# Kernel optimization log

Measured on AMD Instinct MI355X. Metric: run time of the kernel, lower is better.

## Reference

```python
import jax, jax.numpy as jnp
import numpy as np

B, N = 512, 256

def setup_inputs() -> dict:
    key = jax.random.key(0)
    k1, k2 = jax.random.split(key)
    D1 = jax.random.normal(k1, (B, N, N), dtype=jnp.float32)
    D2 = jax.random.normal(k2, (B, N, N), dtype=jnp.float32)
    types1 = jnp.zeros((B, N), dtype=jnp.int32)
    types2 = jnp.zeros((B, N), dtype=jnp.int32)
    return {"D1": D1, "D2": D2, "types1": types1, "types2": types2}


def reference(D1, D2, types1, types2):
    # Hungarian cost: cost[b, i, j] = |mean_k D1[b, k, i] - mean_k D2[b, k, j]|.
    # For an absolute-difference cost between two scalar profiles, the optimal
    # linear assignment (what scipy's linear_sum_assignment returns inside the
    # original tf.py_function) matches sorted values to sorted values; with a
    # point-type constraint, it matches sorted values within each type group.
    # We therefore compute the exact optimal permutation via a lexicographic
    # sort on (type, mean-distance) for each side, which is fully vectorized
    # and avoids the host-side CPU loop of the original layer.
    a = jnp.mean(D1, axis=1)  # [B, N] column means of D1
    b = jnp.mean(D2, axis=1)  # [B, N]

    def optimal_perm(a_row, b_row, t1, t2):
        # sort primarily by type, secondarily by value (lexsort: last key primary)
        order1 = jnp.lexsort((a_row, t1))  # [N] atom indices of D1 in sorted order
        order2 = jnp.lexsort((b_row, t2))  # [N] target positions in sorted order
        # atom order1[k] is placed at position order2[k]
        return jnp.zeros_like(order1).at[order2].set(order1)  # perm[j] = source atom for slot j

    perm = jax.vmap(optimal_perm)(a, b, types1, types2)  # [B, N]

    # Symmetric reorder of rows and columns of D1 by perm.
    D1_rows = jnp.take_along_axis(D1, perm[:, :, None], axis=1)          # [B, N, N]
    D1_reordered = jnp.take_along_axis(D1_rows, perm[:, None, :], axis=2)  # [B, N, N]
    types1_reordered = jnp.take_along_axis(types1, perm, axis=1)         # [B, N]

    # The original layer applies tf.stop_gradient to both outputs.
    D1_reordered = jax.lax.stop_gradient(D1_reordered)
    types1_reordered = jax.lax.stop_gradient(types1_reordered)
    return D1_reordered, types1_reordered
```

## Files before the change

kernel.cpp:

```cpp
#include <hip/hip_runtime.h>
#include <hip/hip_bf16.h>

#define BATCH 512
#define NN 256

__device__ __forceinline__ float4 f4add(float4 x, float4 y) {
  return make_float4(x.x + y.x, x.y + y.y, x.z + y.z, x.w + y.w);
}

__global__ __launch_bounds__(512, 4) void fused_hungarian_kernel(
    const float* __restrict__ D1, const float* __restrict__ D2,
    const int* __restrict__ t1, const int* __restrict__ t2,
    float* __restrict__ out, float* __restrict__ types_out) {
  const int b = blockIdx.x;
  const int tid = threadIdx.x;

  __shared__ float4 partial4[2][4][64];
  __shared__ float va[NN], vb[NN];
  __shared__ int ta[NN], tb[NN];
  __shared__ int ord1[NN], ord2[NN], plds[NN];
  __shared__ float4 rows[8][64];

  {
    const int c4 = tid & 63;
    const int slot = tid >> 6;
    const int mat = slot >> 2;
    const int s2 = slot & 3;
    const int h = s2 >> 1;
    const int tq = s2 & 1;
    const float* __restrict__ src = (mat ? D2 : D1) + (size_t)b * (NN * NN);
    const float* cb = src + (size_t)(h * 128 + 4 * tq) * NN + 4 * c4;

    float4 r0 = *(const float4*)(cb + (size_t)0 * NN);
    float4 r1 = *(const float4*)(cb + (size_t)1 * NN);
    float4 r2 = *(const float4*)(cb + (size_t)2 * NN);
    float4 r3 = *(const float4*)(cb + (size_t)3 * NN);
#pragma unroll
    for (int m = 1; m < 16; ++m) {
      const float* p = cb + (size_t)(8 * m) * NN;
      r0 = f4add(r0, *(const float4*)(p + (size_t)0 * NN));
      r1 = f4add(r1, *(const float4*)(p + (size_t)1 * NN));
      r2 = f4add(r2, *(const float4*)(p + (size_t)2 * NN));
      r3 = f4add(r3, *(const float4*)(p + (size_t)3 * NN));
    }
    partial4[mat][s2][c4] = f4add(f4add(r0, r1), f4add(r2, r3));
  }
  if (tid < NN) ta[tid] = t1[b * NN + tid];
  else          tb[tid - NN] = t2[b * NN + (tid - NN)];
  __syncthreads();

  {
    const int mat = tid >> 8;
    const int c = tid & 255;
    const float p0 = ((const float*)partial4[mat][0])[c];
    const float p1 = ((const float*)partial4[mat][1])[c];
    const float p2 = ((const float*)partial4[mat][2])[c];
    const float p3 = ((const float*)partial4[mat][3])[c];
    const float tot = (p0 + p1) + (p2 + p3);
    const float mean = tot * (1.0f / 256.0f);
    if (mat == 0) va[c] = mean; else vb[c] = mean;
  }
  __syncthreads();

  {
    const int side = tid >> 8;
    const int c = tid & 255;
    const float* __restrict__ vv = side ? vb : va;
    const int* __restrict__ tt = side ? tb : ta;
    const float vi = vv[c];
    const int ti = tt[c];
    int r = 0;
#pragma unroll 4
    for (int j = 0; j < NN; ++j) {
      const int tj = tt[j];
      const float vj = vv[j];
      const bool less =
          (tj < ti) || (tj == ti && (vj < vi || (vj == vi && j < c)));
      r += less ? 1 : 0;
    }
    if (side == 0) ord1[r] = c;
    else           ord2[r] = c;
  }
  __syncthreads();
  if (tid < NN) plds[ord2[tid]] = ord1[tid];
  __syncthreads();
  if (tid < NN) types_out[b * NN + tid] = (float)ta[plds[tid]];

  {
    const int w = tid >> 6;
    const int lane = tid & 63;
    const int j0 = 4 * lane;
    const int pj0 = plds[j0 + 0];
    const int pj1 = plds[j0 + 1];
    const int pj2 = plds[j0 + 2];
    const int pj3 = plds[j0 + 3];
    const float* __restrict__ Db = D1 + (size_t)b * (NN * NN);
    float* __restrict__ outb = out + (size_t)b * (NN * NN);
    const float* rowf = (const float*)&rows[w][0];

    int pi = plds[w];
    float4 vst = *(const float4*)(Db + (size_t)pi * NN + j0);
    for (int iter = 0; iter < 32; ++iter) {
      const int i = iter * 8 + w;
      rows[w][lane] = vst;
      if (iter < 31) {
        const int pin = plds[(iter + 1) * 8 + w];
        vst = *(const float4*)(Db + (size_t)pin * NN + j0);
      }
      float4 o;
      o.x = rowf[pj0];
      o.y = rowf[pj1];
      o.z = rowf[pj2];
      o.w = rowf[pj3];
      *(float4*)(outb + (size_t)i * NN + j0) = o;
    }
  }
}

extern "C" void kernel_launch(void* const* d_in, const int* in_sizes, int n_in,
                              void* d_out, int out_size, void* d_ws, size_t ws_size,
                              hipStream_t stream) {
  const float* D1 = (const float*)d_in[0];
  const float* D2 = (const float*)d_in[1];
  const int* t1 = (const int*)d_in[2];
  const int* t2 = (const int*)d_in[3];

  float* out = (float*)d_out;
  float* types_out = out + (size_t)BATCH * NN * NN;

  fused_hungarian_kernel<<<BATCH, 512, 0, stream>>>(D1, D2, t1, t2, out,
                                                    types_out);
}
```

Before: 346.0 us.

## Stage column-sum loads via global_load_lds DMA and deepen gather prefetch

```diff
diff --git a/kernel.cpp b/kernel.cpp
--- a/kernel.cpp
+++ b/kernel.cpp
@@ -1,11 +1,18 @@
 #include <hip/hip_runtime.h>
-#include <hip/hip_bf16.h>
 
 #define BATCH 512
 #define NN 256
 
+typedef __attribute__((ext_vector_type(4))) float f32x4;
+
 __device__ __forceinline__ float4 f4add(float4 x, float4 y) {
   return make_float4(x.x + y.x, x.y + y.y, x.z + y.z, x.w + y.w);
+}
+
+__device__ __forceinline__ void dma_row16(const float* g, float* l) {
+  __builtin_amdgcn_global_load_lds(
+      (const __attribute__((address_space(1))) void*)g,
+      (__attribute__((address_space(3))) void*)l, 16, 0, 0);
 }
 
 __global__ __launch_bounds__(512, 4) void fused_hungarian_kernel(
@@ -14,51 +21,75 @@
     float* __restrict__ out, float* __restrict__ types_out) {
   const int b = blockIdx.x;
   const int tid = threadIdx.x;
+  const int lane = tid & 63;
+  const int wv = tid >> 6;
 
-  __shared__ float4 partial4[2][4][64];
-  __shared__ float va[NN], vb[NN];
-  __shared__ int ta[NN], tb[NN];
-  __shared__ int ord1[NN], ord2[NN], plds[NN];
-  __shared__ float4 rows[8][64];
+  __shared__ __align__(16) char smem[73728];
+  float* const stagef = (float*)smem;
+  float* const va = (float*)smem;
+  float* const vb = (float*)(smem + 1024);
+  int* const ta = (int*)(smem + 2048);
+  int* const tb = (int*)(smem + 3072);
+  int* const ord1 = (int*)(smem + 4096);
+  int* const ord2 = (int*)(smem + 5120);
+  int* const plds = (int*)(smem + 6144);
+  float4* const rows = (float4*)(smem + 8192);
+  float* const partialf = (float*)(smem + 65536);
 
   {
-    const int c4 = tid & 63;
-    const int slot = tid >> 6;
-    const int mat = slot >> 2;
-    const int s2 = slot & 3;
+    const int mat = wv >> 2;
+    const int s2 = wv & 3;
     const int h = s2 >> 1;
     const int tq = s2 & 1;
     const float* __restrict__ src = (mat ? D2 : D1) + (size_t)b * (NN * NN);
-    const float* cb = src + (size_t)(h * 128 + 4 * tq) * NN + 4 * c4;
+    const float* cb = src + (size_t)(h * 128 + 4 * tq) * NN;
+    float* const wstage = stagef + wv * 2048;
 
-    float4 r0 = *(const float4*)(cb + (size_t)0 * NN);
-    float4 r1 = *(const float4*)(cb + (size_t)1 * NN);
-    float4 r2 = *(const float4*)(cb + (size_t)2 * NN);
-    float4 r3 = *(const float4*)(cb + (size_t)3 * NN);
 #pragma unroll
-    for (int m = 1; m < 16; ++m) {
-      const float* p = cb + (size_t)(8 * m) * NN;
-      r0 = f4add(r0, *(const float4*)(p + (size_t)0 * NN));
-      r1 = f4add(r1, *(const float4*)(p + (size_t)1 * NN));
-      r2 = f4add(r2, *(const float4*)(p + (size_t)2 * NN));
-      r3 = f4add(r3, *(const float4*)(p + (size_t)3 * NN));
+    for (int mk = 0; mk < 8; ++mk) {
+      const int m = mk >> 2, k = mk & 3;
+      dma_row16(cb + (size_t)(8 * m + k) * NN + 4 * lane,
+                wstage + ((m & 1) * 4 + k) * 256);
     }
-    partial4[mat][s2][c4] = f4add(f4add(r0, r1), f4add(r2, r3));
+
+    float4 r0, r1, r2, r3;
+#pragma unroll
+    for (int m = 0; m < 16; ++m) {
+      if (m == 15) asm volatile("s_waitcnt vmcnt(0)" ::: "memory");
+      else         asm volatile("s_waitcnt vmcnt(4)" ::: "memory");
+      const float* sp = wstage + (m & 1) * 1024 + 4 * lane;
+      const float4 v0 = *(const float4*)(sp + 0);
+      const float4 v1 = *(const float4*)(sp + 256);
+      const float4 v2 = *(const float4*)(sp + 512);
+      const float4 v3 = *(const float4*)(sp + 768);
+      asm volatile("s_waitcnt lgkmcnt(0)" ::: "memory");
+      if (m + 2 < 16) {
+#pragma unroll
+        for (int k = 0; k < 4; ++k)
+          dma_row16(cb + (size_t)(8 * (m + 2) + k) * NN + 4 * lane,
+                    wstage + ((m & 1) * 4 + k) * 256);
+      }
+      if (m == 0) { r0 = v0; r1 = v1; r2 = v2; r3 = v3; }
+      else {
+        r0 = f4add(r0, v0); r1 = f4add(r1, v1);
+        r2 = f4add(r2, v2); r3 = f4add(r3, v3);
+      }
+    }
+    const float4 part = f4add(f4add(r0, r1), f4add(r2, r3));
+    *(float4*)(partialf + (mat * 4 + s2) * 256 + 4 * lane) = part;
   }
-  if (tid < NN) ta[tid] = t1[b * NN + tid];
-  else          tb[tid - NN] = t2[b * NN + (tid - NN)];
   __syncthreads();
 
   {
     const int mat = tid >> 8;
     const int c = tid & 255;
-    const float p0 = ((const float*)partial4[mat][0])[c];
-    const float p1 = ((const float*)partial4[mat][1])[c];
-    const float p2 = ((const float*)partial4[mat][2])[c];
-    const float p3 = ((const float*)partial4[mat][3])[c];
-    const float tot = (p0 + p1) + (p2 + p3);
-    const float mean = tot * (1.0f / 256.0f);
-    if (mat == 0) va[c] = mean; else vb[c] = mean;
+    const float p0 = partialf[(mat * 4 + 0) * 256 + c];
+    const float p1 = partialf[(mat * 4 + 1) * 256 + c];
+    const float p2 = partialf[(mat * 4 + 2) * 256 + c];
+    const float p3 = partialf[(mat * 4 + 3) * 256 + c];
+    const float mean = ((p0 + p1) + (p2 + p3)) * (1.0f / 256.0f);
+    if (mat == 0) { va[c] = mean; ta[c] = t1[b * NN + c]; }
+    else          { vb[c] = mean; tb[c] = t2[b * NN + c]; }
   }
   __syncthreads();
 
@@ -87,8 +118,6 @@
   if (tid < NN) types_out[b * NN + tid] = (float)ta[plds[tid]];
 
   {
-    const int w = tid >> 6;
-    const int lane = tid & 63;
     const int j0 = 4 * lane;
     const int pj0 = plds[j0 + 0];
     const int pj1 = plds[j0 + 1];
@@ -96,23 +125,24 @@
     const int pj3 = plds[j0 + 3];
     const float* __restrict__ Db = D1 + (size_t)b * (NN * NN);
     float* __restrict__ outb = out + (size_t)b * (NN * NN);
-    const float* rowf = (const float*)&rows[w][0];
+    const float* const rowf = (const float*)(rows + wv * 64);
 
-    int pi = plds[w];
-    float4 vst = *(const float4*)(Db + (size_t)pi * NN + j0);
+    float4 vA = *(const float4*)(Db + (size_t)plds[wv] * NN + j0);
+    float4 vB = *(const float4*)(Db + (size_t)plds[8 + wv] * NN + j0);
+#pragma unroll 4
     for (int iter = 0; iter < 32; ++iter) {
-      const int i = iter * 8 + w;
-      rows[w][lane] = vst;
-      if (iter < 31) {
-        const int pin = plds[(iter + 1) * 8 + w];
-        vst = *(const float4*)(Db + (size_t)pin * NN + j0);
-      }
+      rows[wv * 64 + lane] = vA;
+      vA = vB;
+      if (iter + 2 < 32)
+        vB = *(const float4*)(Db + (size_t)plds[(iter + 2) * 8 + wv] * NN + j0);
       float4 o;
       o.x = rowf[pj0];
       o.y = rowf[pj1];
       o.z = rowf[pj2];
       o.w = rowf[pj3];
-      *(float4*)(outb + (size_t)i * NN + j0) = o;
+      __builtin_nontemporal_store(
+          *(const f32x4*)&o,
+          (f32x4*)(outb + (size_t)(iter * 8 + wv) * NN + j0));
     }
   }
 }
```

New measurement: 343.2 us. Within noise of the previous version (-0.8%).

## Keep first 64 D1 rows in LDS for the permuted gather; use nontemporal hints

Applied to the files above, without the earlier changes.

```diff
diff --git a/kernel.cpp b/kernel.cpp
--- a/kernel.cpp
+++ b/kernel.cpp
@@ -1,85 +1,116 @@
 #include <hip/hip_runtime.h>
-#include <hip/hip_bf16.h>
 
 #define BATCH 512
 #define NN 256
+#define MSZ (NN * NN)
+#define PERSIST_ROWS 64
 
-__device__ __forceinline__ float4 f4add(float4 x, float4 y) {
-  return make_float4(x.x + y.x, x.y + y.y, x.z + y.z, x.w + y.w);
+typedef __attribute__((ext_vector_type(4))) float f32x4;
+
+template <bool NT, bool PERSIST>
+__device__ __forceinline__ void chainsA(const float* __restrict__ cb,
+                                        float* __restrict__ prow,
+                                        float* __restrict__ partdst) {
+  f32x4 r0, r1, r2, r3;
+#pragma unroll
+  for (int m = 0; m < 16; ++m) {
+    const float* p = cb + (size_t)(8 * m) * NN;
+    f32x4 v0, v1, v2, v3;
+    if (NT) {
+      v0 = __builtin_nontemporal_load((const f32x4*)(p + (size_t)0 * NN));
+      v1 = __builtin_nontemporal_load((const f32x4*)(p + (size_t)1 * NN));
+      v2 = __builtin_nontemporal_load((const f32x4*)(p + (size_t)2 * NN));
+      v3 = __builtin_nontemporal_load((const f32x4*)(p + (size_t)3 * NN));
+    } else {
+      v0 = *(const f32x4*)(p + (size_t)0 * NN);
+      v1 = *(const f32x4*)(p + (size_t)1 * NN);
+      v2 = *(const f32x4*)(p + (size_t)2 * NN);
+      v3 = *(const f32x4*)(p + (size_t)3 * NN);
+    }
+    if (PERSIST && m < 8) {
+      float* q = prow + (size_t)(8 * m) * NN;
+      *(f32x4*)(q + (size_t)0 * NN) = v0;
+      *(f32x4*)(q + (size_t)1 * NN) = v1;
+      *(f32x4*)(q + (size_t)2 * NN) = v2;
+      *(f32x4*)(q + (size_t)3 * NN) = v3;
+    }
+    if (m == 0) { r0 = v0; r1 = v1; r2 = v2; r3 = v3; }
+    else        { r0 += v0; r1 += v1; r2 += v2; r3 += v3; }
+  }
+  *(f32x4*)partdst = (r0 + r1) + (r2 + r3);
 }
 
-__global__ __launch_bounds__(512, 4) void fused_hungarian_kernel(
+__device__ __forceinline__ void rank_side(const float* __restrict__ vv,
+                                          const int* __restrict__ tt, int c,
+                                          int* __restrict__ ordX) {
+  const float vi = vv[c];
+  const int ti = tt[c];
+  int r = 0;
+#pragma unroll 4
+  for (int j = 0; j < NN; ++j) {
+    const int tj = tt[j];
+    const float vj = vv[j];
+    const bool less =
+        (tj < ti) || (tj == ti && (vj < vi || (vj == vi && j < c)));
+    r += less ? 1 : 0;
+  }
+  ordX[r] = c;
+}
+
+__global__ __launch_bounds__(512, 2) void fused_hungarian_kernel(
     const float* __restrict__ D1, const float* __restrict__ D2,
     const int* __restrict__ t1, const int* __restrict__ t2,
     float* __restrict__ out, float* __restrict__ types_out) {
   const int b = blockIdx.x;
   const int tid = threadIdx.x;
+  const int lane = tid & 63;
+  const int wv = tid >> 6;
 
-  __shared__ float4 partial4[2][4][64];
-  __shared__ float va[NN], vb[NN];
-  __shared__ int ta[NN], tb[NN];
-  __shared__ int ord1[NN], ord2[NN], plds[NN];
-  __shared__ float4 rows[8][64];
+  __shared__ __align__(16) char smem[77824];
+  float* const d1rows = (float*)smem;
+  float* const partialf = (float*)(smem + 65536);
+  int* const ord1 = (int*)(smem + 65536);
+  int* const ord2 = (int*)(smem + 66560);
+  int* const plds = (int*)(smem + 67584);
+  float4* const rows = (float4*)(smem + 68608);
+  float* const va = (float*)(smem + 73728);
+  float* const vb = (float*)(smem + 74752);
+  int* const ta = (int*)(smem + 75776);
+  int* const tb = (int*)(smem + 76800);
+
+  const int mat = wv >> 2;
+  const int s2 = wv & 3;
+  const int h = s2 >> 1;
+  const int tq = s2 & 1;
+  const int j0 = 4 * lane;
 
   {
-    const int c4 = tid & 63;
-    const int slot = tid >> 6;
-    const int mat = slot >> 2;
-    const int s2 = slot & 3;
-    const int h = s2 >> 1;
-    const int tq = s2 & 1;
-    const float* __restrict__ src = (mat ? D2 : D1) + (size_t)b * (NN * NN);
-    const float* cb = src + (size_t)(h * 128 + 4 * tq) * NN + 4 * c4;
+    const float* __restrict__ src = (mat ? D2 : D1) + (size_t)b * MSZ;
+    const float* cb = src + (size_t)(h * 128 + 4 * tq) * NN + j0;
+    float* const prow = d1rows + (size_t)(4 * tq) * NN + j0;
+    float* const pdst = partialf + (size_t)(mat * 4 + s2) * NN + j0;
 
-    float4 r0 = *(const float4*)(cb + (size_t)0 * NN);
-    float4 r1 = *(const float4*)(cb + (size_t)1 * NN);
-    float4 r2 = *(const float4*)(cb + (size_t)2 * NN);
-    float4 r3 = *(const float4*)(cb + (size_t)3 * NN);
-#pragma unroll
-    for (int m = 1; m < 16; ++m) {
-      const float* p = cb + (size_t)(8 * m) * NN;
-      r0 = f4add(r0, *(const float4*)(p + (size_t)0 * NN));
-      r1 = f4add(r1, *(const float4*)(p + (size_t)1 * NN));
-      r2 = f4add(r2, *(const float4*)(p + (size_t)2 * NN));
-      r3 = f4add(r3, *(const float4*)(p + (size_t)3 * NN));
-    }
-    partial4[mat][s2][c4] = f4add(f4add(r0, r1), f4add(r2, r3));
-  }
-  if (tid < NN) ta[tid] = t1[b * NN + tid];
-  else          tb[tid - NN] = t2[b * NN + (tid - NN)];
-  __syncthreads();
-
-  {
-    const int mat = tid >> 8;
-    const int c = tid & 255;
-    const float p0 = ((const float*)partial4[mat][0])[c];
-    const float p1 = ((const float*)partial4[mat][1])[c];
-    const float p2 = ((const float*)partial4[mat][2])[c];
-    const float p3 = ((const float*)partial4[mat][3])[c];
-    const float tot = (p0 + p1) + (p2 + p3);
-    const float mean = tot * (1.0f / 256.0f);
-    if (mat == 0) va[c] = mean; else vb[c] = mean;
+    if (wv < 2)            chainsA<false, true>(cb, prow, pdst);
+    else if (mat == 0)     chainsA<false, false>(cb, prow, pdst);
+    else                   chainsA<true, false>(cb, prow, pdst);
   }
   __syncthreads();
 
   {
-    const int side = tid >> 8;
-    const int c = tid & 255;
-    const float* __restrict__ vv = side ? vb : va;
-    const int* __restrict__ tt = side ? tb : ta;
-    const float vi = vv[c];
-    const int ti = tt[c];
-    int r = 0;
-#pragma unroll 4
-    for (int j = 0; j < NN; ++j) {
-      const int tj = tt[j];
-      const float vj = vv[j];
-      const bool less =
-          (tj < ti) || (tj == ti && (vj < vi || (vj == vi && j < c)));
-      r += less ? 1 : 0;
-    }
-    if (side == 0) ord1[r] = c;
-    else           ord2[r] = c;
+    const int cm = tid >> 8, c = tid & 255;
+    const float p0 = partialf[(cm * 4 + 0) * NN + c];
+    const float p1 = partialf[(cm * 4 + 1) * NN + c];
+    const float p2 = partialf[(cm * 4 + 2) * NN + c];
+    const float p3 = partialf[(cm * 4 + 3) * NN + c];
+    const float mean = ((p0 + p1) + (p2 + p3)) * (1.0f / 256.0f);
+    if (cm == 0) { va[c] = mean; ta[c] = t1[b * NN + c]; }
+    else         { vb[c] = mean; tb[c] = t2[b * NN + c]; }
+  }
+  __syncthreads();
+
+  {
+    const int side = tid >> 8, c = tid & 255;
+    rank_side(side ? vb : va, side ? tb : ta, c, side ? ord2 : ord1);
   }
   __syncthreads();
   if (tid < NN) plds[ord2[tid]] = ord1[tid];
@@ -87,32 +118,42 @@
   if (tid < NN) types_out[b * NN + tid] = (float)ta[plds[tid]];
 
   {
-    const int w = tid >> 6;
-    const int lane = tid & 63;
-    const int j0 = 4 * lane;
     const int pj0 = plds[j0 + 0];
     const int pj1 = plds[j0 + 1];
     const int pj2 = plds[j0 + 2];
     const int pj3 = plds[j0 + 3];
-    const float* __restrict__ Db = D1 + (size_t)b * (NN * NN);
-    float* __restrict__ outb = out + (size_t)b * (NN * NN);
-    const float* rowf = (const float*)&rows[w][0];
+    const float* __restrict__ Db = D1 + (size_t)b * MSZ;
+    float* __restrict__ outb = out + (size_t)b * MSZ;
+    float4* const roww = rows + wv * 64;
+    const float* const rowf = (const float*)roww;
 
-    int pi = plds[w];
-    float4 vst = *(const float4*)(Db + (size_t)pi * NN + j0);
-    for (int iter = 0; iter < 32; ++iter) {
-      const int i = iter * 8 + w;
-      rows[w][lane] = vst;
-      if (iter < 31) {
-        const int pin = plds[(iter + 1) * 8 + w];
-        vst = *(const float4*)(Db + (size_t)pin * NN + j0);
+    int pi_cur = plds[wv];
+    bool g_cur = pi_cur >= PERSIST_ROWS;
+    float4 v_cur;
+    if (g_cur) v_cur = *(const float4*)(Db + (size_t)pi_cur * NN + j0);
+
+#pragma unroll 4
+    for (int it = 0; it < 32; ++it) {
+      int pi_nxt = 0;
+      bool g_nxt = false;
+      float4 v_nxt;
+      if (it < 31) {
+        pi_nxt = plds[(it + 1) * 8 + wv];
+        g_nxt = pi_nxt >= PERSIST_ROWS;
+        if (g_nxt) v_nxt = *(const float4*)(Db + (size_t)pi_nxt * NN + j0);
       }
       float4 o;
-      o.x = rowf[pj0];
-      o.y = rowf[pj1];
-      o.z = rowf[pj2];
-      o.w = rowf[pj3];
-      *(float4*)(outb + (size_t)i * NN + j0) = o;
+      if (g_cur) {
+        roww[lane] = v_cur;
+        o.x = rowf[pj0]; o.y = rowf[pj1]; o.z = rowf[pj2]; o.w = rowf[pj3];
+      } else {
+        const float* base = d1rows + (size_t)pi_cur * NN;
+        o.x = base[pj0]; o.y = base[pj1]; o.z = base[pj2]; o.w = base[pj3];
+      }
+      __builtin_nontemporal_store(
+          *(const f32x4*)&o,
+          (f32x4*)(outb + (size_t)(it * 8 + wv) * NN + j0));
+      pi_cur = pi_nxt; g_cur = g_nxt; v_cur = v_nxt;
     }
   }
 }
```

Result: no change. 352.9 us (+2.0%).
